# Kernel tuning notes

Hardware: AMD Instinct MI355X
Metric: run time of the kernel (lower is better)

Reference implementation:

```python
import jax, jax.numpy as jnp
import numpy as np

N_NODES = 50000
N_EDGES = 1600000
H = 128
F_IN = 128
N_CLASSES = 40
N_LAYERS = 8
BETA = 0.1
C_MIN = 0.2
RESIDUAL_WEIGHT = C_MIN - BETA  # 0.1


def setup_inputs() -> dict:
    key = jax.random.key(0)
    ks = jax.random.split(key, 8)
    x = jax.random.normal(ks[0], (N_NODES, F_IN), dtype=jnp.float32)
    edge_index = jax.random.randint(ks[1], (2, N_EDGES), 0, N_NODES, dtype=jnp.int64)
    W_in = jax.random.normal(ks[2], (F_IN, H), dtype=jnp.float32) * 0.05
    b_in = jax.random.normal(ks[3], (H,), dtype=jnp.float32) * 0.05
    gcn_W = jax.random.normal(ks[4], (N_LAYERS, H, H), dtype=jnp.float32) * 0.05
    srelu_b = jax.random.normal(ks[5], (N_LAYERS, H), dtype=jnp.float32) * 0.05
    W_out = jax.random.normal(ks[6], (H, N_CLASSES), dtype=jnp.float32) * 0.05
    b_out = jax.random.normal(ks[7], (N_CLASSES,), dtype=jnp.float32) * 0.05
    return {"x": x, "edge_index": edge_index, "W_in": W_in, "b_in": b_in,
            "gcn_W": gcn_W, "srelu_b": srelu_b, "W_out": W_out, "b_out": b_out}


def _gcn_norm(edge_index, num_nodes, dtype):
    # add_remaining_self_loops: drop existing self loops (zero their weight,
    # keeping static shapes) and append a full set of self loops with weight 1.
    row, col = edge_index[0], edge_index[1]
    w = jnp.where(row == col, 0.0, 1.0).astype(dtype)
    loops = jnp.arange(num_nodes, dtype=edge_index.dtype)
    row_f = jnp.concatenate([row, loops])
    col_f = jnp.concatenate([col, loops])
    w_f = jnp.concatenate([w, jnp.ones((num_nodes,), dtype=dtype)])
    deg = jax.ops.segment_sum(w_f, row_f, num_segments=num_nodes)
    deg_inv_sqrt = jnp.where(deg > 0, deg, 1.0) ** -0.5
    deg_inv_sqrt = jnp.where(deg > 0, deg_inv_sqrt, 0.0)
    norm = deg_inv_sqrt[row_f] * w_f * deg_inv_sqrt[col_f]
    return row_f, col_f, norm


def reference(x, edge_index, W_in, b_in, gcn_W, srelu_b, W_out, b_out):
    n = x.shape[0]
    row_f, col_f, norm = _gcn_norm(edge_index, n, x.dtype)
    # input layer (eval mode: dropout is identity)
    h = jax.nn.relu(x @ W_in + b_in)
    x0 = h

    def layer(h, params):
        W, sb = params
        # degree-normalized gather -> scale -> scatter_add (aggr='add')
        agg = jax.ops.segment_sum(norm[:, None] * h[row_f], col_f, num_segments=n)
        h2 = (1.0 - RESIDUAL_WEIGHT - BETA) * agg + RESIDUAL_WEIGHT * h + BETA * x0
        h2 = h2 @ W
        # SReLU: relu(x - b) + b
        h2 = jax.nn.relu(h2 - sb) + sb
        return h2, None

    h, _ = jax.lax.scan(layer, h, (gcn_W, srelu_b))
    return h @ W_out + b_out
```

## Files before the change

kernel.cpp:

```cpp
#include <hip/hip_runtime.h>

#define N_NODES 50000
#define N_EDGES 1600000
#define HDIM 128
#define N_CLASSES 40
#define N_LAYERS 8
#define CAP 160

#define BUILD_BLOCKS 1563
#define CONV_BLOCKS  3125
#define PREP_BLOCKS   600

typedef _Float16 f16;
typedef _Float16 f16x4 __attribute__((ext_vector_type(4)));
typedef _Float16 f16x8 __attribute__((ext_vector_type(8)));
typedef float f32x4 __attribute__((ext_vector_type(4)));

__device__ __forceinline__ int clamp_idx(int v) {
    v = v < 0 ? 0 : v;
    return v >= N_NODES ? N_NODES - 1 : v;
}


__global__ __launch_bounds__(256) void setup_kernel(
        const int* __restrict__ ei, const float* __restrict__ x,
        const float* __restrict__ W_in, const float* __restrict__ gcn_W,
        const float* __restrict__ W_out,
        int* __restrict__ deg_cnt, int* __restrict__ col_cnt, int* __restrict__ e_slot,
        f16* __restrict__ x16, f16* __restrict__ wt, f16* __restrict__ wot) {
    int b = blockIdx.x;
    if (b < BUILD_BLOCKS) {
        int t = b * 256 + threadIdx.x;
        if (t < N_EDGES / 4) {
            int4 r4 = ((const int4*)ei)[t];
            int4 c4 = ((const int4*)(ei + N_EDGES))[t];
            int rs[4] = {r4.x, r4.y, r4.z, r4.w};
            int cs[4] = {c4.x, c4.y, c4.z, c4.w};
#pragma unroll
            for (int i = 0; i < 4; ++i) {
                int r = clamp_idx(rs[i]);
                int c = clamp_idx(cs[i]);
                if (r != c) {
                    atomicAdd(&deg_cnt[r], 1);
                    int s = atomicAdd(&col_cnt[c], 1);
                    if (s < CAP) e_slot[(size_t)c * CAP + s] = r;
                }
            }
        }
    } else if (b < BUILD_BLOCKS + CONV_BLOCKS) {
        int i = (b - BUILD_BLOCKS) * 256 + threadIdx.x;
        if (i < N_NODES * HDIM / 8) {
            const float4* xs = (const float4*)x;
            float4 v0 = xs[2 * i], v1 = xs[2 * i + 1];
            f16x8 o;
            o[0] = (f16)v0.x; o[1] = (f16)v0.y; o[2] = (f16)v0.z; o[3] = (f16)v0.w;
            o[4] = (f16)v1.x; o[5] = (f16)v1.y; o[6] = (f16)v1.z; o[7] = (f16)v1.w;
            ((f16x8*)x16)[i] = o;
        }
    } else {
        int idx = (b - BUILD_BLOCKS - CONV_BLOCKS) * 256 + threadIdx.x;
        if (idx < 9 * HDIM * HDIM) {
            int mat = idx >> 14;
            int rem = idx & 16383;
            int k = rem >> 7, n = rem & 127;
            float v = (mat == 0) ? W_in[rem] : gcn_W[(mat - 1) * 16384 + rem];
            wt[mat * 16384 + n * 128 + k] = (f16)v;
        } else {
            int j = idx - 9 * HDIM * HDIM;
            if (j < 48 * 128) {
                int n = j >> 7, k = j & 127;
                wot[n * 128 + k] = (n < N_CLASSES) ? (f16)W_out[k * N_CLASSES + n] : (f16)0.f;
            }
        }
    }
}

__global__ void dis_kernel(const int* __restrict__ deg_cnt, float* __restrict__ dis,
                           float* __restrict__ invd) {
    int i = blockIdx.x * blockDim.x + threadIdx.x;
    if (i >= N_NODES) return;
    float d = (float)(deg_cnt[i] + 1);
    dis[i] = rsqrtf(d);
    invd[i] = 1.0f / d;
}


__global__ __launch_bounds__(256) void agg_combine(
        const f16* __restrict__ h16, const f16* __restrict__ h0_16,
        const int* __restrict__ col_cnt, const int* __restrict__ e_slot,
        const float* __restrict__ dis, const float* __restrict__ invd,
        f16* __restrict__ p16) {
    int w = (blockIdx.x * blockDim.x + threadIdx.x) >> 6;
    int lane = threadIdx.x & 63;
    if (w >= N_NODES) return;
    int cnt = col_cnt[w]; if (cnt > CAP) cnt = CAP;
    int half = lane >> 5, m = lane & 31;
    const f16x4* hp = (const f16x4*)h16;
    const int* slots = e_slot + (size_t)w * CAP;
    f32x4 acc = (f32x4){0.f, 0.f, 0.f, 0.f};
    int e = 0;
#pragma unroll 2
    for (; e + 4 <= cnt; e += 4) {
        int4 rr = *(const int4*)(slots + e);
        int ra = half ? rr.y : rr.x;
        int rb = half ? rr.w : rr.z;
        float da = dis[ra], db = dis[rb];
        f16x4 va = hp[(size_t)ra * 32 + m];
        f16x4 vb = hp[(size_t)rb * 32 + m];
#pragma unroll
        for (int c = 0; c < 4; ++c)
            acc[c] += da * (float)va[c] + db * (float)vb[c];
    }
    for (; e < cnt; ++e) {
        if (half == 0) {
            int r = slots[e];
            float d = dis[r];
            f16x4 v = hp[(size_t)r * 32 + m];
#pragma unroll
            for (int c = 0; c < 4; ++c) acc[c] += d * (float)v[c];
        }
    }
#pragma unroll
    for (int c = 0; c < 4; ++c) acc[c] += __shfl_xor(acc[c], 32);

    if (half == 0) {
        float dw = dis[w], iv = invd[w];
        f16x4 hs = hp[(size_t)w * 32 + m];
        f16x4 h0v = ((const f16x4*)h0_16)[(size_t)w * 32 + m];
        f16x4 o;
#pragma unroll
        for (int c = 0; c < 4; ++c) {
            float hv = (float)hs[c];
            float v = 0.8f * (dw * acc[c] + iv * hv) + 0.1f * hv + 0.1f * (float)h0v[c];
            o[c] = (f16)v;
        }
        ((f16x4*)p16)[(size_t)w * 32 + m] = o;
    }
}

#define WT_OFF 16384

__global__ __launch_bounds__(256, 2) void gemm_mfma(
        const f16* __restrict__ A, const f16* __restrict__ Wt,
        const float* __restrict__ bvec, f16* __restrict__ out, int mode) {
    __shared__ uint4 smem4[3072];
    char* smem = (char*)smem4;
    int tid = threadIdx.x;
    int r0 = blockIdx.x * 64;

    const uint4* Asrc = (const uint4*)A;
    for (int c = tid; c < 1024; c += 256) {
        int row = c >> 4, q = c & 15;
        int grow = r0 + row; if (grow >= N_NODES) grow = N_NODES - 1;
        uint4 v = Asrc[(size_t)grow * 16 + q];
        *(uint4*)&smem[row * 256 + ((q * 16) ^ ((row & 7) << 4))] = v;
    }
    const uint4* Wsrc = (const uint4*)Wt;
    for (int c = tid; c < 2048; c += 256) {
        int n = c >> 4, q = c & 15;
        uint4 v = Wsrc[n * 16 + q];
        *(uint4*)&smem[WT_OFF + n * 256 + ((q * 16) ^ ((n & 7) << 4))] = v;
    }
    __syncthreads();

    int l = tid & 63, w = tid >> 6;
    int wr = w >> 1, wc = w & 1;
    int lg = l >> 4, lm = l & 15;

    union F8 { f16x8 v8; struct { f16x4 lo, hi; } p; };
    f32x4 acc[2][4];
#pragma unroll
    for (int m = 0; m < 2; ++m)
#pragma unroll
        for (int j = 0; j < 4; ++j) acc[m][j] = (f32x4){0.f, 0.f, 0.f, 0.f};

#pragma unroll
    for (int kk = 0; kk < 4; ++kk) {
        int boff = kk * 64 + lg * 8;
        F8 a[2], b[4];
#pragma unroll
        for (int m = 0; m < 2; ++m) {
            int row = wr * 32 + m * 16 + lm;
            int swz = (row & 7) << 4;
            int rb = row * 256;
            a[m].p.lo = *(const f16x4*)&smem[rb + (boff ^ swz)];
            a[m].p.hi = *(const f16x4*)&smem[rb + ((boff + 32) ^ swz)];
        }
#pragma unroll
        for (int j = 0; j < 4; ++j) {
            int n = wc * 64 + j * 16 + lm;
            int swz = (n & 7) << 4;
            int nb = WT_OFF + n * 256;
            b[j].p.lo = *(const f16x4*)&smem[nb + (boff ^ swz)];
            b[j].p.hi = *(const f16x4*)&smem[nb + ((boff + 32) ^ swz)];
        }
#pragma unroll
        for (int m = 0; m < 2; ++m)
#pragma unroll
            for (int j = 0; j < 4; ++j)
                acc[m][j] = __builtin_amdgcn_mfma_f32_16x16x32_f16(a[m].v8, b[j].v8, acc[m][j], 0, 0, 0);
    }

#pragma unroll
    for (int m = 0; m < 2; ++m) {
#pragma unroll
        for (int j = 0; j < 4; ++j) {
            int col = wc * 64 + j * 16 + lm;
            float bias = bvec[col];
#pragma unroll
            for (int r = 0; r < 4; ++r) {
                int row = r0 + wr * 32 + m * 16 + lg * 4 + r;
                if (row < N_NODES) {
                    float v = acc[m][j][r];
                    v = mode ? fmaxf(v, bias) : fmaxf(v + bias, 0.f);
                    out[(size_t)row * HDIM + col] = (f16)v;
                }
            }
        }
    }
}

#define WOT_OFF 16384

__global__ __launch_bounds__(256) void out_mfma(
        const f16* __restrict__ A, const f16* __restrict__ Wot,
        const float* __restrict__ bo, float* __restrict__ out) {
    __shared__ uint4 smem4[1792];
    char* smem = (char*)smem4;
    int tid = threadIdx.x;
    int r0 = blockIdx.x * 64;

    const uint4* Asrc = (const uint4*)A;
    for (int c = tid; c < 1024; c += 256) {
        int row = c >> 4, q = c & 15;
        int grow = r0 + row; if (grow >= N_NODES) grow = N_NODES - 1;
        uint4 v = Asrc[(size_t)grow * 16 + q];
        *(uint4*)&smem[row * 256 + ((q * 16) ^ ((row & 7) << 4))] = v;
    }
    const uint4* Wsrc = (const uint4*)Wot;
    for (int c = tid; c < 768; c += 256) {
        int n = c >> 4, q = c & 15;
        uint4 v = Wsrc[n * 16 + q];
        *(uint4*)&smem[WOT_OFF + n * 256 + ((q * 16) ^ ((n & 7) << 4))] = v;
    }
    __syncthreads();

    int l = tid & 63, w = tid >> 6;
    int lg = l >> 4, lm = l & 15;

    union F8 { f16x8 v8; struct { f16x4 lo, hi; } p; };
    f32x4 acc[3];
#pragma unroll
    for (int j = 0; j < 3; ++j) acc[j] = (f32x4){0.f, 0.f, 0.f, 0.f};

#pragma unroll
    for (int kk = 0; kk < 4; ++kk) {
        int boff = kk * 64 + lg * 8;
        F8 a, b[3];
        int row = w * 16 + lm;
        int swz = (row & 7) << 4;
        int rb = row * 256;
        a.p.lo = *(const f16x4*)&smem[rb + (boff ^ swz)];
        a.p.hi = *(const f16x4*)&smem[rb + ((boff + 32) ^ swz)];
#pragma unroll
        for (int j = 0; j < 3; ++j) {
            int n = j * 16 + lm;
            int swz2 = (n & 7) << 4;
            int nb = WOT_OFF + n * 256;
            b[j].p.lo = *(const f16x4*)&smem[nb + (boff ^ swz2)];
            b[j].p.hi = *(const f16x4*)&smem[nb + ((boff + 32) ^ swz2)];
        }
#pragma unroll
        for (int j = 0; j < 3; ++j)
            acc[j] = __builtin_amdgcn_mfma_f32_16x16x32_f16(a.v8, b[j].v8, acc[j], 0, 0, 0);
    }

#pragma unroll
    for (int j = 0; j < 3; ++j) {
        int col = j * 16 + lm;
        if (col < N_CLASSES) {
            float bias = bo[col];
#pragma unroll
            for (int r = 0; r < 4; ++r) {
                int row = r0 + w * 16 + lg * 4 + r;
                if (row < N_NODES)
                    out[(size_t)row * N_CLASSES + col] = acc[j][r] + bias;
            }
        }
    }
}


extern "C" void kernel_launch(void* const* d_in, const int* in_sizes, int n_in,
                              void* d_out, int out_size, void* d_ws, size_t ws_size,
                              hipStream_t stream) {
    const float* x       = (const float*)d_in[0];
    const int*   ei      = (const int*)d_in[1];
    const float* W_in    = (const float*)d_in[2];
    const float* b_in    = (const float*)d_in[3];
    const float* gcn_W   = (const float*)d_in[4];
    const float* srelu_b = (const float*)d_in[5];
    const float* W_out   = (const float*)d_in[6];
    const float* b_out   = (const float*)d_in[7];
    float* outp = (float*)d_out;

    char* ws = (char*)d_ws;
    size_t off = 0;
    auto alloc = [&](size_t bytes) -> void* {
        void* p = ws + off;
        off += (bytes + 255) & ~(size_t)255;
        return p;
    };
    int*   deg_cnt = (int*)alloc((size_t)N_NODES * 4);
    int*   col_cnt = (int*)alloc((size_t)N_NODES * 4);
    float* dis     = (float*)alloc((size_t)N_NODES * 4);
    float* invd    = (float*)alloc((size_t)N_NODES * 4);
    int*   e_slot  = (int*)alloc((size_t)N_NODES * CAP * 4);
    f16*   wt16    = (f16*)alloc((size_t)9 * HDIM * HDIM * 2);
    f16*   wot16   = (f16*)alloc((size_t)48 * HDIM * 2);
    f16*   x16     = (f16*)alloc((size_t)N_NODES * HDIM * 2);
    f16*   h0_16   = (f16*)alloc((size_t)N_NODES * HDIM * 2);
    f16*   hA16    = (f16*)alloc((size_t)N_NODES * HDIM * 2);
    f16*   hB16    = (f16*)alloc((size_t)N_NODES * HDIM * 2);
    f16*   p16     = (f16*)alloc((size_t)N_NODES * HDIM * 2);

    hipMemsetAsync(deg_cnt, 0, (size_t)N_NODES * 4, stream);
    hipMemsetAsync(col_cnt, 0, (size_t)N_NODES * 4, stream);

    setup_kernel<<<BUILD_BLOCKS + CONV_BLOCKS + PREP_BLOCKS, 256, 0, stream>>>(
        ei, x, W_in, gcn_W, W_out, deg_cnt, col_cnt, e_slot, x16, wt16, wot16);
    dis_kernel<<<(N_NODES + 255) / 256, 256, 0, stream>>>(deg_cnt, dis, invd);

    gemm_mfma<<<(N_NODES + 63) / 64, 256, 0, stream>>>(x16, wt16, b_in, h0_16, 0);

    const f16* hcur = h0_16;
    for (int l = 0; l < N_LAYERS; ++l) {
        f16* hnext = (l & 1) ? hB16 : hA16;
        agg_combine<<<(N_NODES * 64 + 255) / 256, 256, 0, stream>>>(
            hcur, h0_16, col_cnt, e_slot, dis, invd, p16);
        gemm_mfma<<<(N_NODES + 63) / 64, 256, 0, stream>>>(
            p16, wt16 + (size_t)(l + 1) * HDIM * HDIM,
            srelu_b + (size_t)l * HDIM, hnext, 1);
        hcur = hnext;
    }

    out_mfma<<<(N_NODES + 63) / 64, 256, 0, stream>>>(hcur, wot16, b_out, outp);
}
```

Baseline: 781.2 us.

## Split node features into four column quarters for cache-local aggregation

Stores all f16 activations as four 32-column planes (quarter-major), so each aggregation pass over one quarter touches a 3.2MB working set that fits better in cache. Aggregation now launches one wave per (quarter, node) with 16 lanes per edge reading 64-byte slices, and 4 edges processed per iteration. GEMM loads and stores are remapped to the new layout, and edge-slot loads/stores use nontemporal hints. The cost is that each node's slot list and dis values are read four times, and the GEMM output writes become narrower and more scattered.

```diff
diff --git a/kernel.cpp b/kernel.cpp
--- a/kernel.cpp
+++ b/kernel.cpp
@@ -11,10 +11,14 @@
 #define CONV_BLOCKS  3125
 #define PREP_BLOCKS   600
 
+#define QF16  ((size_t)N_NODES * 32)
+
 typedef _Float16 f16;
+typedef _Float16 f16x2 __attribute__((ext_vector_type(2)));
 typedef _Float16 f16x4 __attribute__((ext_vector_type(4)));
 typedef _Float16 f16x8 __attribute__((ext_vector_type(8)));
 typedef float f32x4 __attribute__((ext_vector_type(4)));
+typedef int i32x4 __attribute__((ext_vector_type(4)));
 
 __device__ __forceinline__ int clamp_idx(int v) {
     v = v < 0 ? 0 : v;
@@ -32,30 +36,31 @@
     if (b < BUILD_BLOCKS) {
         int t = b * 256 + threadIdx.x;
         if (t < N_EDGES / 4) {
-            int4 r4 = ((const int4*)ei)[t];
-            int4 c4 = ((const int4*)(ei + N_EDGES))[t];
-            int rs[4] = {r4.x, r4.y, r4.z, r4.w};
-            int cs[4] = {c4.x, c4.y, c4.z, c4.w};
+            i32x4 r4 = ((const i32x4*)ei)[t];
+            i32x4 c4 = ((const i32x4*)(ei + N_EDGES))[t];
 #pragma unroll
             for (int i = 0; i < 4; ++i) {
-                int r = clamp_idx(rs[i]);
-                int c = clamp_idx(cs[i]);
+                int r = clamp_idx(r4[i]);
+                int c = clamp_idx(c4[i]);
                 if (r != c) {
                     atomicAdd(&deg_cnt[r], 1);
                     int s = atomicAdd(&col_cnt[c], 1);
-                    if (s < CAP) e_slot[(size_t)c * CAP + s] = r;
+                    if (s < CAP)
+                        __builtin_nontemporal_store(r, &e_slot[(size_t)c * CAP + s]);
                 }
             }
         }
     } else if (b < BUILD_BLOCKS + CONV_BLOCKS) {
         int i = (b - BUILD_BLOCKS) * 256 + threadIdx.x;
         if (i < N_NODES * HDIM / 8) {
+            int node = i >> 4, f8 = i & 15;
             const float4* xs = (const float4*)x;
             float4 v0 = xs[2 * i], v1 = xs[2 * i + 1];
             f16x8 o;
             o[0] = (f16)v0.x; o[1] = (f16)v0.y; o[2] = (f16)v0.z; o[3] = (f16)v0.w;
             o[4] = (f16)v1.x; o[5] = (f16)v1.y; o[6] = (f16)v1.z; o[7] = (f16)v1.w;
-            ((f16x8*)x16)[i] = o;
+            int quarter = f8 >> 2;
+            ((f16x8*)x16)[(size_t)quarter * N_NODES * 4 + (size_t)node * 4 + (f8 & 3)] = o;
         }
     } else {
         int idx = (b - BUILD_BLOCKS - CONV_BLOCKS) * 256 + threadIdx.x;
@@ -90,51 +95,38 @@
         const int* __restrict__ col_cnt, const int* __restrict__ e_slot,
         const float* __restrict__ dis, const float* __restrict__ invd,
         f16* __restrict__ p16) {
-    int w = (blockIdx.x * blockDim.x + threadIdx.x) >> 6;
+    int gw = blockIdx.x * 4 + (threadIdx.x >> 6);
+    int q = gw / N_NODES;
+    int w = gw - q * N_NODES;
     int lane = threadIdx.x & 63;
-    if (w >= N_NODES) return;
+    int g = lane >> 4, m = lane & 15;
     int cnt = col_cnt[w]; if (cnt > CAP) cnt = CAP;
-    int half = lane >> 5, m = lane & 31;
-    const f16x4* hp = (const f16x4*)h16;
+    const f16x2* hq = (const f16x2*)(h16 + (size_t)q * QF16);
     const int* slots = e_slot + (size_t)w * CAP;
-    f32x4 acc = (f32x4){0.f, 0.f, 0.f, 0.f};
-    int e = 0;
+    float a0 = 0.f, a1 = 0.f;
 #pragma unroll 2
-    for (; e + 4 <= cnt; e += 4) {
-        int4 rr = *(const int4*)(slots + e);
-        int ra = half ? rr.y : rr.x;
-        int rb = half ? rr.w : rr.z;
-        float da = dis[ra], db = dis[rb];
-        f16x4 va = hp[(size_t)ra * 32 + m];
-        f16x4 vb = hp[(size_t)rb * 32 + m];
-#pragma unroll
-        for (int c = 0; c < 4; ++c)
-            acc[c] += da * (float)va[c] + db * (float)vb[c];
-    }
-    for (; e < cnt; ++e) {
-        if (half == 0) {
-            int r = slots[e];
-            float d = dis[r];
-            f16x4 v = hp[(size_t)r * 32 + m];
-#pragma unroll
-            for (int c = 0; c < 4; ++c) acc[c] += d * (float)v[c];
-        }
-    }
-#pragma unroll
-    for (int c = 0; c < 4; ++c) acc[c] += __shfl_xor(acc[c], 32);
-
-    if (half == 0) {
+    for (int e = 0; e < cnt; e += 4) {
+        i32x4 rr = __builtin_nontemporal_load((const i32x4*)(slots + e));
+        int r = (g == 0) ? rr.x : (g == 1) ? rr.y : (g == 2) ? rr.z : rr.w;
+        r = clamp_idx(r);
+        float d = dis[r];
+        if (e + g >= cnt) d = 0.f;
+        f16x2 v = hq[(size_t)r * 16 + m];
+        a0 += d * (float)v[0];
+        a1 += d * (float)v[1];
+    }
+    a0 += __shfl_xor(a0, 16); a1 += __shfl_xor(a1, 16);
+    a0 += __shfl_xor(a0, 32); a1 += __shfl_xor(a1, 32);
+
+    if (g == 0) {
         float dw = dis[w], iv = invd[w];
-        f16x4 hs = hp[(size_t)w * 32 + m];
-        f16x4 h0v = ((const f16x4*)h0_16)[(size_t)w * 32 + m];
-        f16x4 o;
-#pragma unroll
-        for (int c = 0; c < 4; ++c) {
-            float hv = (float)hs[c];
-            float v = 0.8f * (dw * acc[c] + iv * hv) + 0.1f * hv + 0.1f * (float)h0v[c];
-            o[c] = (f16)v;
-        }
-        ((f16x4*)p16)[(size_t)w * 32 + m] = o;
+        f16x2 hs = hq[(size_t)w * 16 + m];
+        f16x2 h0v = ((const f16x2*)(h0_16 + (size_t)q * QF16))[(size_t)w * 16 + m];
+        float h0x = (float)hs[0], h0y = (float)hs[1];
+        float vx = 0.8f * (dw * a0 + iv * h0x) + 0.1f * h0x + 0.1f * (float)h0v[0];
+        float vy = 0.8f * (dw * a1 + iv * h0y) + 0.1f * h0y + 0.1f * (float)h0v[1];
+        f16x2 o; o[0] = (f16)vx; o[1] = (f16)vy;
+        ((f16x2*)(p16 + (size_t)q * QF16))[(size_t)w * 16 + m] = o;
     }
 }
 
@@ -150,16 +142,17 @@
 
     const uint4* Asrc = (const uint4*)A;
     for (int c = tid; c < 1024; c += 256) {
-        int row = c >> 4, q = c & 15;
+        int row = c >> 4, s = c & 15;
         int grow = r0 + row; if (grow >= N_NODES) grow = N_NODES - 1;
-        uint4 v = Asrc[(size_t)grow * 16 + q];
-        *(uint4*)&smem[row * 256 + ((q * 16) ^ ((row & 7) << 4))] = v;
+        int quarter = s >> 2;
+        uint4 v = Asrc[(size_t)quarter * N_NODES * 4 + (size_t)grow * 4 + (s & 3)];
+        *(uint4*)&smem[row * 256 + ((s * 16) ^ ((row & 7) << 4))] = v;
     }
     const uint4* Wsrc = (const uint4*)Wt;
     for (int c = tid; c < 2048; c += 256) {
-        int n = c >> 4, q = c & 15;
-        uint4 v = Wsrc[n * 16 + q];
-        *(uint4*)&smem[WT_OFF + n * 256 + ((q * 16) ^ ((n & 7) << 4))] = v;
+        int n = c >> 4, s = c & 15;
+        uint4 v = Wsrc[n * 16 + s];
+        *(uint4*)&smem[WT_OFF + n * 256 + ((s * 16) ^ ((n & 7) << 4))] = v;
     }
     __syncthreads();
 
@@ -207,13 +200,15 @@
         for (int j = 0; j < 4; ++j) {
             int col = wc * 64 + j * 16 + lm;
             float bias = bvec[col];
+            int quarter = col >> 5, cm = col & 31;
+            f16* outq = out + (size_t)quarter * QF16;
 #pragma unroll
             for (int r = 0; r < 4; ++r) {
                 int row = r0 + wr * 32 + m * 16 + lg * 4 + r;
                 if (row < N_NODES) {
                     float v = acc[m][j][r];
                     v = mode ? fmaxf(v, bias) : fmaxf(v + bias, 0.f);
-                    out[(size_t)row * HDIM + col] = (f16)v;
+                    outq[(size_t)row * 32 + cm] = (f16)v;
                 }
             }
         }
@@ -232,16 +227,17 @@
 
     const uint4* Asrc = (const uint4*)A;
     for (int c = tid; c < 1024; c += 256) {
-        int row = c >> 4, q = c & 15;
+        int row = c >> 4, s = c & 15;
         int grow = r0 + row; if (grow >= N_NODES) grow = N_NODES - 1;
-        uint4 v = Asrc[(size_t)grow * 16 + q];
-        *(uint4*)&smem[row * 256 + ((q * 16) ^ ((row & 7) << 4))] = v;
+        int quarter = s >> 2;
+        uint4 v = Asrc[(size_t)quarter * N_NODES * 4 + (size_t)grow * 4 + (s & 3)];
+        *(uint4*)&smem[row * 256 + ((s * 16) ^ ((row & 7) << 4))] = v;
     }
     const uint4* Wsrc = (const uint4*)Wot;
     for (int c = tid; c < 768; c += 256) {
-        int n = c >> 4, q = c & 15;
-        uint4 v = Wsrc[n * 16 + q];
-        *(uint4*)&smem[WOT_OFF + n * 256 + ((q * 16) ^ ((n & 7) << 4))] = v;
+        int n = c >> 4, s = c & 15;
+        uint4 v = Wsrc[n * 16 + s];
+        *(uint4*)&smem[WOT_OFF + n * 256 + ((s * 16) ^ ((n & 7) << 4))] = v;
     }
     __syncthreads();
 
@@ -336,7 +332,7 @@
     const f16* hcur = h0_16;
     for (int l = 0; l < N_LAYERS; ++l) {
         f16* hnext = (l & 1) ? hB16 : hA16;
-        agg_combine<<<(N_NODES * 64 + 255) / 256, 256, 0, stream>>>(
+        agg_combine<<<N_NODES, 256, 0, stream>>>(
             hcur, h0_16, col_cnt, e_slot, dis, invd, p16);
         gemm_mfma<<<(N_NODES + 63) / 64, 256, 0, stream>>>(
             p16, wt16 + (size_t)(l + 1) * HDIM * HDIM,
```

After: 1.748 ms. 124% more time.

## Store degree-prescaled features, use 16-bit neighbor indices, simplify gather loop

Applied to the files above, without the earlier changes.

Layer outputs are now stored premultiplied by the node's inverse-sqrt degree, so the aggregation no longer loads a per-neighbor degree scale. The combine step uses precomputed per-node coefficients packed in a float4, and the output GEMM undoes the scaling. Neighbor slot indices shrink to 16-bit, and each lane now handles two features over full 64-lane rows instead of splitting edges across half-waves. Storing scaled values in fp16 changes rounding. A 16-bit index cannot represent node IDs up to 49999 above 65535, so it fits here. The gather also issues narrower 4-byte loads per lane.

```diff
diff --git a/kernel.cpp b/kernel.cpp
--- a/kernel.cpp
+++ b/kernel.cpp
@@ -12,9 +12,11 @@
 #define PREP_BLOCKS   600
 
 typedef _Float16 f16;
+typedef _Float16 f16x2 __attribute__((ext_vector_type(2)));
 typedef _Float16 f16x4 __attribute__((ext_vector_type(4)));
 typedef _Float16 f16x8 __attribute__((ext_vector_type(8)));
 typedef float f32x4 __attribute__((ext_vector_type(4)));
+typedef int i32x4 __attribute__((ext_vector_type(4)));
 
 __device__ __forceinline__ int clamp_idx(int v) {
     v = v < 0 ? 0 : v;
@@ -26,24 +28,23 @@
         const int* __restrict__ ei, const float* __restrict__ x,
         const float* __restrict__ W_in, const float* __restrict__ gcn_W,
         const float* __restrict__ W_out,
-        int* __restrict__ deg_cnt, int* __restrict__ col_cnt, int* __restrict__ e_slot,
+        int* __restrict__ deg_cnt, int* __restrict__ col_cnt,
+        unsigned short* __restrict__ e_slot,
         f16* __restrict__ x16, f16* __restrict__ wt, f16* __restrict__ wot) {
     int b = blockIdx.x;
     if (b < BUILD_BLOCKS) {
         int t = b * 256 + threadIdx.x;
         if (t < N_EDGES / 4) {
-            int4 r4 = ((const int4*)ei)[t];
-            int4 c4 = ((const int4*)(ei + N_EDGES))[t];
-            int rs[4] = {r4.x, r4.y, r4.z, r4.w};
-            int cs[4] = {c4.x, c4.y, c4.z, c4.w};
+            i32x4 r4 = ((const i32x4*)ei)[t];
+            i32x4 c4 = ((const i32x4*)(ei + N_EDGES))[t];
 #pragma unroll
             for (int i = 0; i < 4; ++i) {
-                int r = clamp_idx(rs[i]);
-                int c = clamp_idx(cs[i]);
+                int r = clamp_idx(r4[i]);
+                int c = clamp_idx(c4[i]);
                 if (r != c) {
                     atomicAdd(&deg_cnt[r], 1);
                     int s = atomicAdd(&col_cnt[c], 1);
-                    if (s < CAP) e_slot[(size_t)c * CAP + s] = r;
+                    if (s < CAP) e_slot[(size_t)c * CAP + s] = (unsigned short)r;
                 }
             }
         }
@@ -75,74 +76,58 @@
     }
 }
 
-__global__ void dis_kernel(const int* __restrict__ deg_cnt, float* __restrict__ dis,
-                           float* __restrict__ invd) {
+__global__ void combo_kernel(const int* __restrict__ deg_cnt, float4* __restrict__ combo) {
     int i = blockIdx.x * blockDim.x + threadIdx.x;
     if (i >= N_NODES) return;
     float d = (float)(deg_cnt[i] + 1);
-    dis[i] = rsqrtf(d);
-    invd[i] = 1.0f / d;
+    float dis = rsqrtf(d);
+    float g = sqrtf(d);
+    combo[i] = make_float4(dis, 0.8f * dis, (0.8f / d + 0.1f) * g, g);
 }
 
 
 __global__ __launch_bounds__(256) void agg_combine(
-        const f16* __restrict__ h16, const f16* __restrict__ h0_16,
-        const int* __restrict__ col_cnt, const int* __restrict__ e_slot,
-        const float* __restrict__ dis, const float* __restrict__ invd,
-        f16* __restrict__ p16) {
+        const f16* __restrict__ hs, const f16* __restrict__ h0_16,
+        const int* __restrict__ col_cnt, const unsigned short* __restrict__ e_slot,
+        const float4* __restrict__ combo, f16* __restrict__ p16) {
     int w = (blockIdx.x * blockDim.x + threadIdx.x) >> 6;
     int lane = threadIdx.x & 63;
     if (w >= N_NODES) return;
     int cnt = col_cnt[w]; if (cnt > CAP) cnt = CAP;
-    int half = lane >> 5, m = lane & 31;
-    const f16x4* hp = (const f16x4*)h16;
-    const int* slots = e_slot + (size_t)w * CAP;
-    f32x4 acc = (f32x4){0.f, 0.f, 0.f, 0.f};
+    const f16x2* hp = (const f16x2*)hs;
+    const unsigned short* slots = e_slot + (size_t)w * CAP;
+    float ax = 0.f, ay = 0.f;
     int e = 0;
-#pragma unroll 2
     for (; e + 4 <= cnt; e += 4) {
-        int4 rr = *(const int4*)(slots + e);
-        int ra = half ? rr.y : rr.x;
-        int rb = half ? rr.w : rr.z;
-        float da = dis[ra], db = dis[rb];
-        f16x4 va = hp[(size_t)ra * 32 + m];
-        f16x4 vb = hp[(size_t)rb * 32 + m];
-#pragma unroll
-        for (int c = 0; c < 4; ++c)
-            acc[c] += da * (float)va[c] + db * (float)vb[c];
+        ushort4 s4 = *(const ushort4*)(slots + e);
+        f16x2 v0 = hp[(size_t)s4.x * 64 + lane];
+        f16x2 v1 = hp[(size_t)s4.y * 64 + lane];
+        f16x2 v2 = hp[(size_t)s4.z * 64 + lane];
+        f16x2 v3 = hp[(size_t)s4.w * 64 + lane];
+        ax += (float)v0[0] + (float)v1[0] + (float)v2[0] + (float)v3[0];
+        ay += (float)v0[1] + (float)v1[1] + (float)v2[1] + (float)v3[1];
     }
     for (; e < cnt; ++e) {
-        if (half == 0) {
-            int r = slots[e];
-            float d = dis[r];
-            f16x4 v = hp[(size_t)r * 32 + m];
-#pragma unroll
-            for (int c = 0; c < 4; ++c) acc[c] += d * (float)v[c];
-        }
-    }
-#pragma unroll
-    for (int c = 0; c < 4; ++c) acc[c] += __shfl_xor(acc[c], 32);
-
-    if (half == 0) {
-        float dw = dis[w], iv = invd[w];
-        f16x4 hs = hp[(size_t)w * 32 + m];
-        f16x4 h0v = ((const f16x4*)h0_16)[(size_t)w * 32 + m];
-        f16x4 o;
-#pragma unroll
-        for (int c = 0; c < 4; ++c) {
-            float hv = (float)hs[c];
-            float v = 0.8f * (dw * acc[c] + iv * hv) + 0.1f * hv + 0.1f * (float)h0v[c];
-            o[c] = (f16)v;
-        }
-        ((f16x4*)p16)[(size_t)w * 32 + m] = o;
-    }
+        int r = slots[e];
+        f16x2 v = hp[(size_t)r * 64 + lane];
+        ax += (float)v[0];
+        ay += (float)v[1];
+    }
+    float4 cb = combo[w];
+    f16x2 hw = hp[(size_t)w * 64 + lane];
+    f16x2 h0v = ((const f16x2*)h0_16)[(size_t)w * 64 + lane];
+    float px = cb.y * ax + cb.z * (float)hw[0] + 0.1f * (float)h0v[0];
+    float py = cb.y * ay + cb.z * (float)hw[1] + 0.1f * (float)h0v[1];
+    f16x2 o; o[0] = (f16)px; o[1] = (f16)py;
+    ((f16x2*)p16)[(size_t)w * 64 + lane] = o;
 }
 
 #define WT_OFF 16384
 
 __global__ __launch_bounds__(256, 2) void gemm_mfma(
         const f16* __restrict__ A, const f16* __restrict__ Wt,
-        const float* __restrict__ bvec, f16* __restrict__ out, int mode) {
+        const float* __restrict__ bvec, const float4* __restrict__ combo,
+        f16* __restrict__ hs_out, f16* __restrict__ h0_out, int mode) {
     __shared__ uint4 smem4[3072];
     char* smem = (char*)smem4;
     int tid = threadIdx.x;
@@ -204,16 +189,18 @@
 #pragma unroll
     for (int m = 0; m < 2; ++m) {
 #pragma unroll
-        for (int j = 0; j < 4; ++j) {
-            int col = wc * 64 + j * 16 + lm;
-            float bias = bvec[col];
-#pragma unroll
-            for (int r = 0; r < 4; ++r) {
-                int row = r0 + wr * 32 + m * 16 + lg * 4 + r;
-                if (row < N_NODES) {
+        for (int r = 0; r < 4; ++r) {
+            int row = r0 + wr * 32 + m * 16 + lg * 4 + r;
+            if (row < N_NODES) {
+                float dis = combo[row].x;
+#pragma unroll
+                for (int j = 0; j < 4; ++j) {
+                    int col = wc * 64 + j * 16 + lm;
+                    float bias = bvec[col];
                     float v = acc[m][j][r];
                     v = mode ? fmaxf(v, bias) : fmaxf(v + bias, 0.f);
-                    out[(size_t)row * HDIM + col] = (f16)v;
+                    if (mode == 0) h0_out[(size_t)row * HDIM + col] = (f16)v;
+                    hs_out[(size_t)row * HDIM + col] = (f16)(dis * v);
                 }
             }
         }
@@ -224,7 +211,8 @@
 
 __global__ __launch_bounds__(256) void out_mfma(
         const f16* __restrict__ A, const f16* __restrict__ Wot,
-        const float* __restrict__ bo, float* __restrict__ out) {
+        const float* __restrict__ bo, const float4* __restrict__ combo,
+        float* __restrict__ out) {
     __shared__ uint4 smem4[1792];
     char* smem = (char*)smem4;
     int tid = threadIdx.x;
@@ -276,15 +264,15 @@
     }
 
 #pragma unroll
-    for (int j = 0; j < 3; ++j) {
-        int col = j * 16 + lm;
-        if (col < N_CLASSES) {
-            float bias = bo[col];
-#pragma unroll
-            for (int r = 0; r < 4; ++r) {
-                int row = r0 + w * 16 + lg * 4 + r;
-                if (row < N_NODES)
-                    out[(size_t)row * N_CLASSES + col] = acc[j][r] + bias;
+    for (int r = 0; r < 4; ++r) {
+        int row = r0 + w * 16 + lg * 4 + r;
+        if (row < N_NODES) {
+            float g = combo[row].w;
+#pragma unroll
+            for (int j = 0; j < 3; ++j) {
+                int col = j * 16 + lm;
+                if (col < N_CLASSES)
+                    out[(size_t)row * N_CLASSES + col] = g * acc[j][r] + bo[col];
             }
         }
     }
@@ -311,38 +299,39 @@
         off += (bytes + 255) & ~(size_t)255;
         return p;
     };
-    int*   deg_cnt = (int*)alloc((size_t)N_NODES * 4);
-    int*   col_cnt = (int*)alloc((size_t)N_NODES * 4);
-    float* dis     = (float*)alloc((size_t)N_NODES * 4);
-    float* invd    = (float*)alloc((size_t)N_NODES * 4);
-    int*   e_slot  = (int*)alloc((size_t)N_NODES * CAP * 4);
-    f16*   wt16    = (f16*)alloc((size_t)9 * HDIM * HDIM * 2);
-    f16*   wot16   = (f16*)alloc((size_t)48 * HDIM * 2);
-    f16*   x16     = (f16*)alloc((size_t)N_NODES * HDIM * 2);
-    f16*   h0_16   = (f16*)alloc((size_t)N_NODES * HDIM * 2);
-    f16*   hA16    = (f16*)alloc((size_t)N_NODES * HDIM * 2);
-    f16*   hB16    = (f16*)alloc((size_t)N_NODES * HDIM * 2);
-    f16*   p16     = (f16*)alloc((size_t)N_NODES * HDIM * 2);
+    int*    deg_cnt = (int*)alloc((size_t)N_NODES * 4);
+    int*    col_cnt = (int*)alloc((size_t)N_NODES * 4);
+    float4* combo   = (float4*)alloc((size_t)N_NODES * 16);
+    unsigned short* e_slot = (unsigned short*)alloc((size_t)N_NODES * CAP * 2);
+    f16*    wt16    = (f16*)alloc((size_t)9 * HDIM * HDIM * 2);
+    f16*    wot16   = (f16*)alloc((size_t)48 * HDIM * 2);
+    f16*    x16     = (f16*)alloc((size_t)N_NODES * HDIM * 2);
+    f16*    h0_16   = (f16*)alloc((size_t)N_NODES * HDIM * 2);
+    f16*    hs0     = (f16*)alloc((size_t)N_NODES * HDIM * 2);
+    f16*    hsA     = (f16*)alloc((size_t)N_NODES * HDIM * 2);
+    f16*    hsB     = (f16*)alloc((size_t)N_NODES * HDIM * 2);
+    f16*    p16     = (f16*)alloc((size_t)N_NODES * HDIM * 2);
 
     hipMemsetAsync(deg_cnt, 0, (size_t)N_NODES * 4, stream);
     hipMemsetAsync(col_cnt, 0, (size_t)N_NODES * 4, stream);
 
     setup_kernel<<<BUILD_BLOCKS + CONV_BLOCKS + PREP_BLOCKS, 256, 0, stream>>>(
         ei, x, W_in, gcn_W, W_out, deg_cnt, col_cnt, e_slot, x16, wt16, wot16);
-    dis_kernel<<<(N_NODES + 255) / 256, 256, 0, stream>>>(deg_cnt, dis, invd);
-
-    gemm_mfma<<<(N_NODES + 63) / 64, 256, 0, stream>>>(x16, wt16, b_in, h0_16, 0);
-
-    const f16* hcur = h0_16;
+    combo_kernel<<<(N_NODES + 255) / 256, 256, 0, stream>>>(deg_cnt, combo);
+
+    gemm_mfma<<<(N_NODES + 63) / 64, 256, 0, stream>>>(
+        x16, wt16, b_in, combo, hs0, h0_16, 0);
+
+    const f16* hcur = hs0;
     for (int l = 0; l < N_LAYERS; ++l) {
-        f16* hnext = (l & 1) ? hB16 : hA16;
+        f16* hnext = (l & 1) ? hsB : hsA;
         agg_combine<<<(N_NODES * 64 + 255) / 256, 256, 0, stream>>>(
-            hcur, h0_16, col_cnt, e_slot, dis, invd, p16);
+            hcur, h0_16, col_cnt, e_slot, combo, p16);
         gemm_mfma<<<(N_NODES + 63) / 64, 256, 0, stream>>>(
             p16, wt16 + (size_t)(l + 1) * HDIM * HDIM,
-            srelu_b + (size_t)l * HDIM, hnext, 1);
+            srelu_b + (size_t)l * HDIM, combo, hnext, nullptr, 1);
         hcur = hnext;
     }
 
-    out_mfma<<<(N_NODES + 63) / 64, 256, 0, stream>>>(hcur, wot16, b_out, outp);
-}
+    out_mfma<<<(N_NODES + 63) / 64, 256, 0, stream>>>(hcur, wot16, b_out, combo, outp);
+}
```

Result: slower. 834.0 us (+6.8%).
